# Kernel optimization log

Hardware: AMD Instinct MI355X
Metric: run time of the kernel (lower is better)

## Reference

```python
import jax, jax.numpy as jnp
import numpy as np

HIDDEN = 1024
RANK = 4
INPUT = 16
ALPHA = 0.1
BASE_SCALE = 500.0
B = 32
T = 1024


def setup_inputs() -> dict:
    key = jax.random.key(0)
    k1, k2, k3, k4 = jax.random.split(key, 4)
    std = HIDDEN ** -0.25  # matches cov ~ I/sqrt(hidden) in original init
    x = jax.random.normal(k1, (B, T, INPUT), dtype=jnp.float32)
    m = jax.random.normal(k2, (HIDDEN, RANK), dtype=jnp.float32) * std
    n = jax.random.normal(k3, (HIDDEN, RANK), dtype=jnp.float32) * std
    I_mat = jax.random.normal(k4, (HIDDEN, INPUT), dtype=jnp.float32) * std
    return {"x": x, "m": m, "n": n, "I_mat": I_mat}


def reference(x, m, n, I_mat):
    # J = (m @ n.T) * base_scale / hidden ; recurrent term (J @ tanh(h).T).T
    # == tanh(h) @ J.T == ((tanh(h) @ n) @ m.T) * scale  (low-rank form, same math)
    scale = BASE_SCALE / HIDDEN

    def step(h, x_t):
        rec = (jnp.tanh(h) @ n) @ m.T * scale          # [B, H]
        dh = -h + rec + x_t @ I_mat.T                  # [B, H]
        h = h + ALPHA * dh
        return h, h

    h0 = jnp.zeros((x.shape[0], HIDDEN), dtype=x.dtype)
    _, hiddens = jax.lax.scan(step, h0, jnp.swapaxes(x, 0, 1))  # [T, B, H]
    hiddens = jnp.swapaxes(hiddens, 0, 1)                       # [B, T, H]

    span = jnp.concatenate([m, I_mat], axis=1)   # [H, RANK+INPUT]
    proj = jnp.linalg.pinv(span)                 # [RANK+INPUT, H]
    # (pinv(span) @ hiddens.permute(0,2,1)).permute(0,2,1)
    return jnp.einsum('ph,bth->btp', proj, hiddens)  # [B, T, RANK+INPUT]
```

## Files before the change

kernel.cpp:

```cpp
#include <hip/hip_runtime.h>
#include <math.h>

#define HIDDEN_ 1024
#define RANK_ 4
#define INPUT_ 16
#define T_ 1024
#define BATCH_ 32

#define NTHREADS_ 256
#define NWAVES_ (NTHREADS_ / 64)
#define EPT_ (HIDDEN_ / NTHREADS_)
#define CH_ 64
#define NCH_ (T_ / CH_)

#define PRE_BLOCKS_ 2048
#define ROWS_ (BATCH_ * T_)
#define PASSES_ (ROWS_ / PRE_BLOCKS_)

typedef float f32x4 __attribute__((ext_vector_type(4)));

__device__ __forceinline__ float fast_exp2(float x) {
#if defined(__has_builtin)
#if __has_builtin(__builtin_amdgcn_exp2f)
    return __builtin_amdgcn_exp2f(x);
#else
    return exp2f(x);
#endif
#else
    return exp2f(x);
#endif
}

__device__ __forceinline__ float fast_rcp(float x) {
#if defined(__has_builtin)
#if __has_builtin(__builtin_amdgcn_rcpf)
    return __builtin_amdgcn_rcpf(x);
#else
    return 1.0f / x;
#endif
#else
    return 1.0f / x;
#endif
}

__device__ __forceinline__ float tanh_fast(float x) {
    float e = fast_exp2(x * 2.885390081777926815f);
    return fmaf(-2.0f, fast_rcp(e + 1.0f), 1.0f);
}

#define DPP_ADD(v, ctrl)                                                          \
    do {                                                                          \
        int _t = __builtin_amdgcn_update_dpp(0, __float_as_int(v), (ctrl), 0xf,   \
                                             0xf, true);                          \
        (v) += __int_as_float(_t);                                                \
    } while (0)

__global__ __launch_bounds__(NTHREADS_, 2) void precompute_u(
    const float* __restrict__ x,
    const float* __restrict__ imat,
    float* __restrict__ u)
{
    const int tid = threadIdx.x;
    const int bid = blockIdx.x;
    const float kin = 0.1f;

    float Ir[4][INPUT_];
#pragma unroll
    for (int r = 0; r < 4; ++r) {
        const float* ip = imat + (4 * tid + r) * INPUT_;
#pragma unroll
        for (int q = 0; q < 4; ++q) {
            const float4 v = *(const float4*)(ip + 4 * q);
            Ir[r][q*4+0] = kin * v.x; Ir[r][q*4+1] = kin * v.y;
            Ir[r][q*4+2] = kin * v.z; Ir[r][q*4+3] = kin * v.w;
        }
    }

    for (int p = 0; p < PASSES_; ++p) {
        const int row = p * PRE_BLOCKS_ + bid;
        const float* xr = x + (size_t)row * INPUT_;
        float xv[INPUT_];
#pragma unroll
        for (int q = 0; q < 4; ++q) {
            const float4 v = ((const float4*)xr)[q];
            xv[q*4+0] = v.x; xv[q*4+1] = v.y; xv[q*4+2] = v.z; xv[q*4+3] = v.w;
        }
        float4 acc;
        float a[4];
#pragma unroll
        for (int r = 0; r < 4; ++r) {
            float s0 = xv[0] * Ir[r][0];
            float s1 = xv[1] * Ir[r][1];
#pragma unroll
            for (int i = 2; i < INPUT_; i += 2) {
                s0 = fmaf(xv[i],     Ir[r][i],     s0);
                s1 = fmaf(xv[i + 1], Ir[r][i + 1], s1);
            }
            a[r] = s0 + s1;
        }
        acc.x = a[0]; acc.y = a[1]; acc.z = a[2]; acc.w = a[3];
        *(float4*)(u + (size_t)row * HIDDEN_ + 4 * tid) = acc;
    }
}

__global__ __launch_bounds__(NTHREADS_)
__attribute__((amdgpu_waves_per_eu(1, 1)))
void rnn_scan_kernel(
    const float* __restrict__ x,
    const float* __restrict__ m,
    const float* __restrict__ n,
    const float* __restrict__ u,
    float* __restrict__ out)
{
    const int b    = blockIdx.x;
    const int tid  = threadIdx.x;
    const int wave = tid >> 6;
    const int lane = tid & 63;

    const float kd   = 0.9f;
    const float krec = 0.1f * (500.0f / 1024.0f);

    float h[EPT_];
    float mrs[EPT_][RANK_];
    float nr[EPT_][RANK_];
#pragma unroll
    for (int j = 0; j < EPT_; ++j) {
        const int hidx = tid * EPT_ + j;
        h[j] = 0.0f;
        const float4 mv = *(const float4*)(m + hidx * RANK_);
        mrs[j][0] = krec * mv.x; mrs[j][1] = krec * mv.y;
        mrs[j][2] = krec * mv.z; mrs[j][3] = krec * mv.w;
        const float4 nv = *(const float4*)(n + hidx * RANK_);
        nr[j][0] = nv.x; nr[j][1] = nv.y; nr[j][2] = nv.z; nr[j][3] = nv.w;
    }

    __shared__ float4 part[2][NWAVES_];
    __shared__ float xs[2][CH_ * INPUT_];

    const float* xb = x + (size_t)b * T_ * INPUT_;
    const float* ub = u + (size_t)b * T_ * HIDDEN_ + tid * EPT_;
    float* ob = out + (size_t)b * T_ * (RANK_ + INPUT_);

    {
        float4 c0 = *(const float4*)(xb + tid * 4);
        *(float4*)&xs[0][tid * 4] = c0;
    }
    float4 xstage = *(const float4*)(xb + CH_ * INPUT_ + tid * 4);

    float4 upf[4];
#pragma unroll
    for (int k = 0; k < 4; ++k)
        upf[k] = *(const float4*)(ub + (size_t)k * HIDDEN_);

    float y = 0.0f;
    const int yoff = (tid >= 4 && tid < 20) ? (tid - 4) : 0;

#pragma unroll 4
    for (int t = 0; t < T_; ++t) {
        float th[EPT_];
#pragma unroll
        for (int j = 0; j < EPT_; ++j) th[j] = tanh_fast(h[j]);

        float p0 = th[0] * nr[0][0], p1 = th[0] * nr[0][1];
        float p2 = th[0] * nr[0][2], p3 = th[0] * nr[0][3];
#pragma unroll
        for (int j = 1; j < EPT_; ++j) {
            p0 = fmaf(th[j], nr[j][0], p0);
            p1 = fmaf(th[j], nr[j][1], p1);
            p2 = fmaf(th[j], nr[j][2], p2);
            p3 = fmaf(th[j], nr[j][3], p3);
        }

        DPP_ADD(p0, 0x111); DPP_ADD(p1, 0x111); DPP_ADD(p2, 0x111); DPP_ADD(p3, 0x111);
        DPP_ADD(p0, 0x112); DPP_ADD(p1, 0x112); DPP_ADD(p2, 0x112); DPP_ADD(p3, 0x112);
        DPP_ADD(p0, 0x114); DPP_ADD(p1, 0x114); DPP_ADD(p2, 0x114); DPP_ADD(p3, 0x114);
        DPP_ADD(p0, 0x118); DPP_ADD(p1, 0x118); DPP_ADD(p2, 0x118); DPP_ADD(p3, 0x118);
        DPP_ADD(p0, 0x142); DPP_ADD(p1, 0x142); DPP_ADD(p2, 0x142); DPP_ADD(p3, 0x142);
        DPP_ADD(p0, 0x143); DPP_ADD(p1, 0x143); DPP_ADD(p2, 0x143); DPP_ADD(p3, 0x143);

        if (lane == 63) part[t & 1][wave] = make_float4(p0, p1, p2, p3);

        asm volatile("s_waitcnt lgkmcnt(0)\n\ts_barrier" ::: "memory");

        if ((t & (CH_ - 1)) == 0) {
            const int c = t >> 6;
            *(float4*)&xs[(c + 1) & 1][tid * 4] = xstage;
            const int cl = (c + 2 < NCH_) ? (c + 2) : (NCH_ - 1);
            xstage = *(const float4*)(xb + cl * CH_ * INPUT_ + tid * 4);
        }

        const float4 q0 = part[t & 1][0];
        const float4 q1 = part[t & 1][1];
        const float4 q2 = part[t & 1][2];
        const float4 q3 = part[t & 1][3];
        const float xyv = xs[(t >> 6) & 1][(t & 63) * INPUT_ + yoff];

        const float4 uv = upf[t & 3];
        {
            const int tn = (t + 4 < T_) ? (t + 4) : t;
            upf[t & 3] = *(const float4*)(ub + (size_t)tn * HIDDEN_);
        }

        const float s0 = (q0.x + q1.x) + (q2.x + q3.x);
        const float s1 = (q0.y + q1.y) + (q2.y + q3.y);
        const float s2 = (q0.z + q1.z) + (q2.z + q3.z);
        const float s3 = (q0.w + q1.w) + (q2.w + q3.w);

        const float uq[4] = {uv.x, uv.y, uv.z, uv.w};
#pragma unroll
        for (int j = 0; j < EPT_; ++j) {
            float a01 = fmaf(s1, mrs[j][1], fmaf(s0, mrs[j][0], uq[j]));
            float a23 = fmaf(s3, mrs[j][3], s2 * mrs[j][2]);
            h[j] = fmaf(kd, h[j], a01 + a23);
        }

        if (tid < 20) {
            float drive;
            if (tid < 4) {
                float sv = (tid == 0) ? s0 : (tid == 1) ? s1 : (tid == 2) ? s2 : s3;
                drive = krec * sv;
            } else {
                drive = 0.1f * xyv;
            }
            y = fmaf(kd, y, drive);
            ob[t * 20 + tid] = y;
        }
    }
}

__global__ __launch_bounds__(NTHREADS_)
__attribute__((amdgpu_waves_per_eu(1, 1)))
void rnn_scan_fallback(
    const float* __restrict__ x, const float* __restrict__ m,
    const float* __restrict__ n, const float* __restrict__ imat,
    float* __restrict__ out)
{
    const int b    = blockIdx.x;
    const int tid  = threadIdx.x;
    const int wave = tid >> 6;
    const int lane = tid & 63;
    const float kd = 0.9f, krec = 0.1f * (500.0f / 1024.0f), kin = 0.1f;

    float h[EPT_], mrs[EPT_][RANK_], nr[EPT_][RANK_], Irs[EPT_][INPUT_];
#pragma unroll
    for (int j = 0; j < EPT_; ++j) {
        const int hidx = tid * EPT_ + j;
        h[j] = 0.0f;
        const float4 mv = *(const float4*)(m + hidx * RANK_);
        mrs[j][0] = krec * mv.x; mrs[j][1] = krec * mv.y;
        mrs[j][2] = krec * mv.z; mrs[j][3] = krec * mv.w;
        const float4 nv = *(const float4*)(n + hidx * RANK_);
        nr[j][0] = nv.x; nr[j][1] = nv.y; nr[j][2] = nv.z; nr[j][3] = nv.w;
#pragma unroll
        for (int q = 0; q < 4; ++q) {
            const float4 iv = *(const float4*)(imat + hidx * INPUT_ + q * 4);
            Irs[j][q*4+0] = kin * iv.x; Irs[j][q*4+1] = kin * iv.y;
            Irs[j][q*4+2] = kin * iv.z; Irs[j][q*4+3] = kin * iv.w;
        }
    }
    __shared__ float4 part[2][NWAVES_];
    __shared__ float xs[2][CH_ * INPUT_];
    const float* xb = x + (size_t)b * T_ * INPUT_;
    float* ob = out + (size_t)b * T_ * (RANK_ + INPUT_);
    {
        float4 c0 = *(const float4*)(xb + tid * 4);
        *(float4*)&xs[0][tid * 4] = c0;
    }
    float4 xstage = *(const float4*)(xb + CH_ * INPUT_ + tid * 4);
    float y = 0.0f;
    const int yoff = (tid >= 4 && tid < 20) ? (tid - 4) : 0;

    for (int t = 0; t < T_; ++t) {
        float th[EPT_];
#pragma unroll
        for (int j = 0; j < EPT_; ++j) th[j] = tanh_fast(h[j]);
        float p0 = th[0] * nr[0][0], p1 = th[0] * nr[0][1];
        float p2 = th[0] * nr[0][2], p3 = th[0] * nr[0][3];
#pragma unroll
        for (int j = 1; j < EPT_; ++j) {
            p0 = fmaf(th[j], nr[j][0], p0); p1 = fmaf(th[j], nr[j][1], p1);
            p2 = fmaf(th[j], nr[j][2], p2); p3 = fmaf(th[j], nr[j][3], p3);
        }
        DPP_ADD(p0, 0x111); DPP_ADD(p1, 0x111); DPP_ADD(p2, 0x111); DPP_ADD(p3, 0x111);
        DPP_ADD(p0, 0x112); DPP_ADD(p1, 0x112); DPP_ADD(p2, 0x112); DPP_ADD(p3, 0x112);
        DPP_ADD(p0, 0x114); DPP_ADD(p1, 0x114); DPP_ADD(p2, 0x114); DPP_ADD(p3, 0x114);
        DPP_ADD(p0, 0x118); DPP_ADD(p1, 0x118); DPP_ADD(p2, 0x118); DPP_ADD(p3, 0x118);
        DPP_ADD(p0, 0x142); DPP_ADD(p1, 0x142); DPP_ADD(p2, 0x142); DPP_ADD(p3, 0x142);
        DPP_ADD(p0, 0x143); DPP_ADD(p1, 0x143); DPP_ADD(p2, 0x143); DPP_ADD(p3, 0x143);
        if (lane == 63) part[t & 1][wave] = make_float4(p0, p1, p2, p3);
        asm volatile("s_waitcnt lgkmcnt(0)\n\ts_barrier" ::: "memory");
        if ((t & (CH_ - 1)) == 0) {
            const int c = t >> 6;
            *(float4*)&xs[(c + 1) & 1][tid * 4] = xstage;
            const int cl = (c + 2 < NCH_) ? (c + 2) : (NCH_ - 1);
            xstage = *(const float4*)(xb + cl * CH_ * INPUT_ + tid * 4);
        }
        const float* xsp = &xs[(t >> 6) & 1][(t & 63) * INPUT_];
        const float4 xa = ((const float4*)xsp)[0];
        const float4 xbv = ((const float4*)xsp)[1];
        const float4 xc = ((const float4*)xsp)[2];
        const float4 xd = ((const float4*)xsp)[3];
        const float xyv = xsp[yoff];
        const float4 q0 = part[t & 1][0];
        const float4 q1 = part[t & 1][1];
        const float4 q2 = part[t & 1][2];
        const float4 q3 = part[t & 1][3];
        float ax[EPT_];
#pragma unroll
        for (int j = 0; j < EPT_; ++j) {
            float a = xa.x * Irs[j][0];
            float c = xa.y * Irs[j][1];
            a = fmaf(xa.z, Irs[j][2], a);   c = fmaf(xa.w, Irs[j][3], c);
            a = fmaf(xbv.x, Irs[j][4], a);  c = fmaf(xbv.y, Irs[j][5], c);
            a = fmaf(xbv.z, Irs[j][6], a);  c = fmaf(xbv.w, Irs[j][7], c);
            a = fmaf(xc.x, Irs[j][8], a);   c = fmaf(xc.y, Irs[j][9], c);
            a = fmaf(xc.z, Irs[j][10], a);  c = fmaf(xc.w, Irs[j][11], c);
            a = fmaf(xd.x, Irs[j][12], a);  c = fmaf(xd.y, Irs[j][13], c);
            a = fmaf(xd.z, Irs[j][14], a);  c = fmaf(xd.w, Irs[j][15], c);
            ax[j] = a + c;
        }
        const float s0 = (q0.x + q1.x) + (q2.x + q3.x);
        const float s1 = (q0.y + q1.y) + (q2.y + q3.y);
        const float s2 = (q0.z + q1.z) + (q2.z + q3.z);
        const float s3 = (q0.w + q1.w) + (q2.w + q3.w);
#pragma unroll
        for (int j = 0; j < EPT_; ++j) {
            float a01 = fmaf(s1, mrs[j][1], fmaf(s0, mrs[j][0], ax[j]));
            float a23 = fmaf(s3, mrs[j][3], s2 * mrs[j][2]);
            h[j] = fmaf(kd, h[j], a01 + a23);
        }
        if (tid < 20) {
            float drive;
            if (tid < 4) {
                float sv = (tid == 0) ? s0 : (tid == 1) ? s1 : (tid == 2) ? s2 : s3;
                drive = krec * sv;
            } else {
                drive = kin * xyv;
            }
            y = fmaf(kd, y, drive);
            ob[t * 20 + tid] = y;
        }
    }
}

extern "C" void kernel_launch(void* const* d_in, const int* in_sizes, int n_in,
                              void* d_out, int out_size, void* d_ws, size_t ws_size,
                              hipStream_t stream) {
    const float* x    = (const float*)d_in[0];
    const float* m    = (const float*)d_in[1];
    const float* n    = (const float*)d_in[2];
    const float* imat = (const float*)d_in[3];
    float* out = (float*)d_out;

    const size_t u_bytes = (size_t)BATCH_ * T_ * HIDDEN_ * sizeof(float);
    if (d_ws != nullptr && ws_size >= u_bytes) {
        float* u = (float*)d_ws;
        precompute_u<<<dim3(PRE_BLOCKS_), dim3(NTHREADS_), 0, stream>>>(x, imat, u);
        rnn_scan_kernel<<<dim3(BATCH_), dim3(NTHREADS_), 0, stream>>>(x, m, n, u, out);
    } else {
        rnn_scan_fallback<<<dim3(BATCH_), dim3(NTHREADS_), 0, stream>>>(x, m, n, imat, out);
    }
}
```

Baseline: 570.4 us.

## Pack two batch elements into each 512-thread scan block

The scan kernel now runs two independent batch recurrences per block: each 256-thread half handles one batch, with its own shared-memory partial-sum and x staging buffers. The grid is halved and occupancy is raised to two waves per EU. The aim is to interleave two latency-bound recurrences on one CU so each hides the other's stalls. In exchange, both halves share one block barrier, which couples their progress, and only half as many CUs are used.

```diff
diff --git a/kernel.cpp b/kernel.cpp
--- a/kernel.cpp
+++ b/kernel.cpp
@@ -7,9 +7,10 @@
 #define T_ 1024
 #define BATCH_ 32
 
-#define NTHREADS_ 256
-#define NWAVES_ (NTHREADS_ / 64)
-#define EPT_ (HIDDEN_ / NTHREADS_)
+#define SCAN_THREADS_ 512
+#define TPB_ 256
+#define NWAVES_H_ (TPB_ / 64)
+#define EPT_ (HIDDEN_ / TPB_)
 #define CH_ 64
 #define NCH_ (T_ / CH_)
 
@@ -55,7 +56,7 @@
         (v) += __int_as_float(_t);                                                \
     } while (0)
 
-__global__ __launch_bounds__(NTHREADS_, 2) void precompute_u(
+__global__ __launch_bounds__(TPB_, 2) void precompute_u(
     const float* __restrict__ x,
     const float* __restrict__ imat,
     float* __restrict__ u)
@@ -103,8 +104,8 @@
     }
 }
 
-__global__ __launch_bounds__(NTHREADS_)
-__attribute__((amdgpu_waves_per_eu(1, 1)))
+__global__ __launch_bounds__(SCAN_THREADS_)
+__attribute__((amdgpu_waves_per_eu(2, 2)))
 void rnn_scan_kernel(
     const float* __restrict__ x,
     const float* __restrict__ m,
@@ -112,10 +113,12 @@
     const float* __restrict__ u,
     float* __restrict__ out)
 {
-    const int b    = blockIdx.x;
     const int tid  = threadIdx.x;
-    const int wave = tid >> 6;
+    const int half = tid >> 8;
+    const int tidh = tid & (TPB_ - 1);
+    const int wv   = tidh >> 6;
     const int lane = tid & 63;
+    const int b    = blockIdx.x * 2 + half;
 
     const float kd   = 0.9f;
     const float krec = 0.1f * (500.0f / 1024.0f);
@@ -125,7 +128,7 @@
     float nr[EPT_][RANK_];
 #pragma unroll
     for (int j = 0; j < EPT_; ++j) {
-        const int hidx = tid * EPT_ + j;
+        const int hidx = tidh * EPT_ + j;
         h[j] = 0.0f;
         const float4 mv = *(const float4*)(m + hidx * RANK_);
         mrs[j][0] = krec * mv.x; mrs[j][1] = krec * mv.y;
@@ -134,18 +137,18 @@
         nr[j][0] = nv.x; nr[j][1] = nv.y; nr[j][2] = nv.z; nr[j][3] = nv.w;
     }
 
-    __shared__ float4 part[2][NWAVES_];
-    __shared__ float xs[2][CH_ * INPUT_];
+    __shared__ float4 part[2][2][NWAVES_H_];
+    __shared__ float xs[2][2][CH_ * INPUT_];
 
     const float* xb = x + (size_t)b * T_ * INPUT_;
-    const float* ub = u + (size_t)b * T_ * HIDDEN_ + tid * EPT_;
+    const float* ub = u + (size_t)b * T_ * HIDDEN_ + tidh * EPT_;
     float* ob = out + (size_t)b * T_ * (RANK_ + INPUT_);
 
     {
-        float4 c0 = *(const float4*)(xb + tid * 4);
-        *(float4*)&xs[0][tid * 4] = c0;
-    }
-    float4 xstage = *(const float4*)(xb + CH_ * INPUT_ + tid * 4);
+        float4 c0 = *(const float4*)(xb + tidh * 4);
+        *(float4*)&xs[half][0][tidh * 4] = c0;
+    }
+    float4 xstage = *(const float4*)(xb + CH_ * INPUT_ + tidh * 4);
 
     float4 upf[4];
 #pragma unroll
@@ -153,7 +156,7 @@
         upf[k] = *(const float4*)(ub + (size_t)k * HIDDEN_);
 
     float y = 0.0f;
-    const int yoff = (tid >= 4 && tid < 20) ? (tid - 4) : 0;
+    const int yoff = (tidh >= 4 && tidh < 20) ? (tidh - 4) : 0;
 
 #pragma unroll 4
     for (int t = 0; t < T_; ++t) {
@@ -178,22 +181,22 @@
         DPP_ADD(p0, 0x142); DPP_ADD(p1, 0x142); DPP_ADD(p2, 0x142); DPP_ADD(p3, 0x142);
         DPP_ADD(p0, 0x143); DPP_ADD(p1, 0x143); DPP_ADD(p2, 0x143); DPP_ADD(p3, 0x143);
 
-        if (lane == 63) part[t & 1][wave] = make_float4(p0, p1, p2, p3);
+        if (lane == 63) part[half][t & 1][wv] = make_float4(p0, p1, p2, p3);
 
         asm volatile("s_waitcnt lgkmcnt(0)\n\ts_barrier" ::: "memory");
 
         if ((t & (CH_ - 1)) == 0) {
             const int c = t >> 6;
-            *(float4*)&xs[(c + 1) & 1][tid * 4] = xstage;
+            *(float4*)&xs[half][(c + 1) & 1][tidh * 4] = xstage;
             const int cl = (c + 2 < NCH_) ? (c + 2) : (NCH_ - 1);
-            xstage = *(const float4*)(xb + cl * CH_ * INPUT_ + tid * 4);
-        }
-
-        const float4 q0 = part[t & 1][0];
-        const float4 q1 = part[t & 1][1];
-        const float4 q2 = part[t & 1][2];
-        const float4 q3 = part[t & 1][3];
-        const float xyv = xs[(t >> 6) & 1][(t & 63) * INPUT_ + yoff];
+            xstage = *(const float4*)(xb + cl * CH_ * INPUT_ + tidh * 4);
+        }
+
+        const float4 q0 = part[half][t & 1][0];
+        const float4 q1 = part[half][t & 1][1];
+        const float4 q2 = part[half][t & 1][2];
+        const float4 q3 = part[half][t & 1][3];
+        const float xyv = xs[half][(t >> 6) & 1][(t & 63) * INPUT_ + yoff];
 
         const float4 uv = upf[t & 3];
         {
@@ -214,21 +217,21 @@
             h[j] = fmaf(kd, h[j], a01 + a23);
         }
 
-        if (tid < 20) {
+        if (tidh < 20) {
             float drive;
-            if (tid < 4) {
-                float sv = (tid == 0) ? s0 : (tid == 1) ? s1 : (tid == 2) ? s2 : s3;
+            if (tidh < 4) {
+                float sv = (tidh == 0) ? s0 : (tidh == 1) ? s1 : (tidh == 2) ? s2 : s3;
                 drive = krec * sv;
             } else {
                 drive = 0.1f * xyv;
             }
             y = fmaf(kd, y, drive);
-            ob[t * 20 + tid] = y;
-        }
-    }
-}
-
-__global__ __launch_bounds__(NTHREADS_)
+            ob[t * 20 + tidh] = y;
+        }
+    }
+}
+
+__global__ __launch_bounds__(TPB_)
 __attribute__((amdgpu_waves_per_eu(1, 1)))
 void rnn_scan_fallback(
     const float* __restrict__ x, const float* __restrict__ m,
@@ -258,7 +261,7 @@
             Irs[j][q*4+2] = kin * iv.z; Irs[j][q*4+3] = kin * iv.w;
         }
     }
-    __shared__ float4 part[2][NWAVES_];
+    __shared__ float4 part[2][NWAVES_H_];
     __shared__ float xs[2][CH_ * INPUT_];
     const float* xb = x + (size_t)b * T_ * INPUT_;
     float* ob = out + (size_t)b * T_ * (RANK_ + INPUT_);
@@ -355,9 +358,9 @@
     const size_t u_bytes = (size_t)BATCH_ * T_ * HIDDEN_ * sizeof(float);
     if (d_ws != nullptr && ws_size >= u_bytes) {
         float* u = (float*)d_ws;
-        precompute_u<<<dim3(PRE_BLOCKS_), dim3(NTHREADS_), 0, stream>>>(x, imat, u);
-        rnn_scan_kernel<<<dim3(BATCH_), dim3(NTHREADS_), 0, stream>>>(x, m, n, u, out);
+        precompute_u<<<dim3(PRE_BLOCKS_), dim3(TPB_), 0, stream>>>(x, imat, u);
+        rnn_scan_kernel<<<dim3(BATCH_ / 2), dim3(SCAN_THREADS_), 0, stream>>>(x, m, n, u, out);
     } else {
-        rnn_scan_fallback<<<dim3(BATCH_), dim3(NTHREADS_), 0, stream>>>(x, m, n, imat, out);
-    }
-}
+        rnn_scan_fallback<<<dim3(BATCH_), dim3(TPB_), 0, stream>>>(x, m, n, imat, out);
+    }
+}
```

After: 699.2 us. +22.6%, slower.
